# Kernel optimization log

Hardware: AMD Instinct MI355X
Metric: run time of the kernel (lower is better)

Reference implementation:

```python
import jax, jax.numpy as jnp
import numpy as np

B, S, H, I, G = 2, 1024, 1024, 4096, 8


def setup_inputs() -> dict:
    key = jax.random.key(0)
    k1, k2, k3, k4 = jax.random.split(key, 4)
    # kaiming-style scaled init (scale matters only for numerics, not math)
    hidden_states = jax.random.normal(k1, (B, S, H), dtype=jnp.float32)
    WG = jax.random.normal(k2, (H, G), dtype=jnp.float32) * (1.0 / np.sqrt(H))
    Wi = jax.random.normal(k3, (G, H, I), dtype=jnp.float32) * (1.0 / np.sqrt(H))
    down = jax.random.normal(k4, (I, H), dtype=jnp.float32) * (1.0 / np.sqrt(I))
    return {"hidden_states": hidden_states, "WG": WG, "Wi": Wi, "down": down, "topk": 2}


def topk_sigmoid(gate, k):
    # gate: [B,S,G] -> sigmoid gated scores masked to top-k per token
    _, idx = jax.lax.top_k(gate, k)                       # idx: [B,S,k]
    mask = (idx[..., None] == jnp.arange(gate.shape[-1])).any(axis=-2)  # [B,S,G] bool
    return jax.nn.sigmoid(gate) * mask


def reference(hidden_states, WG, Wi, down, topk):
    gate = hidden_states @ WG                             # [B,S,G]
    g = topk_sigmoid(gate, topk)                          # [B,S,G]
    # dense contraction over all groups (faithful to original einsum)
    up = jnp.einsum('bse,bsg,geo->bso', hidden_states, g, Wi)  # [B,S,I]
    act = jnp.square(jax.nn.relu(up))                     # ReLU^2
    return act @ down                                     # [B,S,H]
```

## Files before the change

kernel.cpp:

```cpp
#include <hip/hip_runtime.h>
#include <hip/hip_bf16.h>

typedef unsigned short u16;
typedef short short8_t __attribute__((ext_vector_type(8)));
typedef float f32x4 __attribute__((ext_vector_type(4)));

#define GLOBAL_AS(p) ((const __attribute__((address_space(1))) void*)(p))
#define LDS_AS(p)    ((__attribute__((address_space(3))) void*)(p))

__device__ __forceinline__ u16 f2bf(float f) {
    union { float f; unsigned int u; } x;
    x.f = f;
    unsigned int r = x.u + 0x7fffu + ((x.u >> 16) & 1u);
    return (u16)(r >> 16);
}

#define M_NMT   0
#define M_TE    2
#define M_TB    42
#define M_PAIR  96
#define M_RTOK  4192
#define M_RW    9312

__global__ __launch_bounds__(64) void gate_topk_kernel(
    const float* __restrict__ h, const float* __restrict__ wg, float* __restrict__ w) {
    const int t = blockIdx.x;
    const int lane = threadIdx.x;
    float acc[8];
#pragma unroll
    for (int g = 0; g < 8; ++g) acc[g] = 0.f;
    for (int e = lane; e < 1024; e += 64) {
        float hv = h[(size_t)t * 1024 + e];
        float4 r0 = *(const float4*)&wg[e * 8];
        float4 r1 = *(const float4*)&wg[e * 8 + 4];
        acc[0] += hv * r0.x; acc[1] += hv * r0.y; acc[2] += hv * r0.z; acc[3] += hv * r0.w;
        acc[4] += hv * r1.x; acc[5] += hv * r1.y; acc[6] += hv * r1.z; acc[7] += hv * r1.w;
    }
#pragma unroll
    for (int off = 32; off > 0; off >>= 1) {
#pragma unroll
        for (int g = 0; g < 8; ++g) acc[g] += __shfl_down(acc[g], off);
    }
    if (lane == 0) {
        int i1 = 0;
        for (int g = 1; g < 8; ++g) if (acc[g] > acc[i1]) i1 = g;
        int i2 = -1;
        for (int g = 0; g < 8; ++g) {
            if (g == i1) continue;
            if (i2 < 0 || acc[g] > acc[i2]) i2 = g;
        }
#pragma unroll
        for (int g = 0; g < 8; ++g) {
            float v = (g == i1 || g == i2) ? (1.f / (1.f + __expf(-acc[g]))) : 0.f;
            w[t * 8 + g] = v;
        }
    }
}

__global__ __launch_bounds__(256) void scan_kernel(
    const float* __restrict__ w, int* __restrict__ meta) {
    __shared__ int cnt[8], pos[8];
    const int tid = threadIdx.x;
    if (tid < 8) cnt[tid] = 0;
    __syncthreads();
    for (int t = tid; t < 2048; t += 256) {
#pragma unroll
        for (int g = 0; g < 8; ++g)
            if (w[t * 8 + g] > 0.f) atomicAdd(&cnt[g], 1);
    }
    __syncthreads();
    if (tid == 0) {
        int base = 0, mt = 0;
        for (int e = 0; e < 8; ++e) {
            pos[e] = base;
            int nt = (cnt[e] + 127) >> 7;
            for (int k = 0; k < nt; ++k) { meta[M_TE + mt] = e; meta[M_TB + mt] = base + k * 128; ++mt; }
            base += nt << 7;
        }
        meta[M_NMT] = mt;
        meta[1] = base;
    }
    __syncthreads();
    for (int i = tid; i < 5120; i += 256) meta[M_RTOK + i] = -1;
    __syncthreads();
    float* row_w = (float*)&meta[M_RW];
    for (int t = tid; t < 2048; t += 256) {
        int slot = 0;
#pragma unroll
        for (int g = 0; g < 8; ++g) {
            float wv = w[t * 8 + g];
            if (wv > 0.f) {
                int p = atomicAdd(&pos[g], 1);
                meta[M_RTOK + p] = t;
                row_w[p] = wv;
                meta[M_PAIR + t * 2 + slot] = p;
                ++slot;
            }
        }
    }
}

__global__ __launch_bounds__(256) void gather_a_kernel(
    const float* __restrict__ h, const int* __restrict__ meta, u16* __restrict__ A) {
    const int row = blockIdx.x;
    const int tid = threadIdx.x;
    const int tok = meta[M_RTOK + row];
    u16* dst = A + (size_t)row * 1024;
    if (tok < 0) {
        uint2 z; z.x = 0u; z.y = 0u;
        ((uint2*)dst)[tid] = z;
        return;
    }
    const float wv = ((const float*)&meta[M_RW])[row];
    float4 v = ((const float4*)(h + (size_t)tok * 1024))[tid];
    u16 o[4] = { f2bf(v.x * wv), f2bf(v.y * wv), f2bf(v.z * wv), f2bf(v.w * wv) };
    ((uint2*)dst)[tid] = *(const uint2*)o;
}

__global__ __launch_bounds__(256) void gemm1_sparse_kernel(
    const u16* __restrict__ A, const float* __restrict__ Wi,
    float* __restrict__ up, const int* __restrict__ meta) {
    const int mt = blockIdx.y;
    if (mt >= meta[M_NMT]) return;
    const int e = meta[M_TE + mt];
    const int base = meta[M_TB + mt];
    const int n0 = blockIdx.x * 128;
    const int K = 1024, N = 4096;
    const float* Bm = Wi + (size_t)e * K * N;

    __shared__ short a_tile[128 * 64];
    __shared__ short b_tile[128 * 64];
    const int tid = threadIdx.x;
    const int lane = tid & 63;
    const int wave = tid >> 6;
    const int wm = (wave >> 1) * 64;
    const int wn = (wave & 1) * 64;
    const int r = lane & 15;
    const int quad = lane >> 4;
    const int rowin = lane >> 3;
    const int achk = ((lane & 7) ^ (rowin & 7)) * 8;
    const int aldst = (lane & 7) * 8;

    const f32x4 vzero = {0.f, 0.f, 0.f, 0.f};
    f32x4 acc[4][4];
#pragma unroll
    for (int i = 0; i < 4; ++i)
#pragma unroll
        for (int j = 0; j < 4; ++j) acc[i][j] = vzero;

    for (int kb = 0; kb < K; kb += 64) {
        float bv[4][8];
#pragma unroll
        for (int cb = 0; cb < 4; ++cb) {
            int idx = cb * 256 + tid;
            int bn_ = idx & 127;
            int bk8 = idx >> 7;
            const float* bp = Bm + (size_t)(kb + bk8 * 8) * N + n0 + bn_;
#pragma unroll
            for (int kk = 0; kk < 8; ++kk) bv[cb][kk] = bp[(size_t)kk * N];
        }
        __syncthreads();
#pragma unroll
        for (int it = 0; it < 4; ++it) {
            int row = wave * 8 + it * 32 + rowin;
            const u16* ga = A + (size_t)(base + row) * K + kb + achk;
            __builtin_amdgcn_global_load_lds(GLOBAL_AS(ga), LDS_AS(&a_tile[row * 64 + aldst]), 16, 0, 0);
        }
#pragma unroll
        for (int cb = 0; cb < 4; ++cb) {
            int idx = cb * 256 + tid;
            int bn_ = idx & 127;
            int bk8 = idx >> 7;
            u16 bc[8];
#pragma unroll
            for (int kk = 0; kk < 8; ++kk) bc[kk] = f2bf(bv[cb][kk]);
            *(short8_t*)&b_tile[bn_ * 64 + ((bk8 ^ (bn_ & 7)) * 8)] = *(const short8_t*)bc;
        }
        __syncthreads();
#pragma unroll
        for (int ks = 0; ks < 2; ++ks) {
            const int cp = ((ks * 4 + quad) ^ (r & 7)) * 8;
            short8_t af[4], bfr[4];
#pragma unroll
            for (int i = 0; i < 4; ++i)
                af[i] = *(const short8_t*)&a_tile[(wm + i * 16 + r) * 64 + cp];
#pragma unroll
            for (int j = 0; j < 4; ++j)
                bfr[j] = *(const short8_t*)&b_tile[(wn + j * 16 + r) * 64 + cp];
#pragma unroll
            for (int i = 0; i < 4; ++i)
#pragma unroll
                for (int j = 0; j < 4; ++j)
                    acc[i][j] = __builtin_amdgcn_mfma_f32_16x16x32_bf16(af[i], bfr[j], acc[i][j], 0, 0, 0);
        }
        __syncthreads();
    }
#pragma unroll
    for (int i = 0; i < 4; ++i)
#pragma unroll
        for (int j = 0; j < 4; ++j)
#pragma unroll
            for (int reg = 0; reg < 4; ++reg) {
                int cr = base + wm + i * 16 + quad * 4 + reg;
                int cc = n0 + wn + j * 16 + r;
                up[(size_t)cr * N + cc] = acc[i][j][reg];
            }
}

__global__ __launch_bounds__(256) void combine_kernel(
    const float* __restrict__ up, const int* __restrict__ meta, u16* __restrict__ act) {
    const int t = blockIdx.x;
    const int tid = threadIdx.x;
    const int p0 = meta[M_PAIR + t * 2];
    const int p1 = meta[M_PAIR + t * 2 + 1];
    const float* r0 = up + (size_t)p0 * 4096;
    const float* r1 = up + (size_t)p1 * 4096;
    u16* dst = act + (size_t)t * 4096;
#pragma unroll
    for (int it = 0; it < 4; ++it) {
        int i = (tid + it * 256) * 4;
        float4 a = *(const float4*)&r0[i];
        float4 b = *(const float4*)&r1[i];
        float s0 = a.x + b.x, s1 = a.y + b.y, s2 = a.z + b.z, s3 = a.w + b.w;
        s0 = s0 > 0.f ? s0 * s0 : 0.f;
        s1 = s1 > 0.f ? s1 * s1 : 0.f;
        s2 = s2 > 0.f ? s2 * s2 : 0.f;
        s3 = s3 > 0.f ? s3 * s3 : 0.f;
        u16 o[4] = { f2bf(s0), f2bf(s1), f2bf(s2), f2bf(s3) };
        *(uint2*)&dst[i] = *(const uint2*)o;
    }
}

__global__ __launch_bounds__(256) void transpose_cvt_kernel(
    const float* __restrict__ in, u16* __restrict__ out, int R, int C) {
    __shared__ u16 tile[64][65];
    const int rt = blockIdx.y * 64;
    const int ct = blockIdx.x * 64;
    const int tid = threadIdx.x;
#pragma unroll
    for (int it = 0; it < 2; ++it) {
        int r = (tid >> 3) + it * 32;
        int c8 = (tid & 7) * 8;
        const float* ip = &in[(size_t)(rt + r) * C + ct + c8];
        float4 v0 = *(const float4*)ip;
        float4 v1 = *(const float4*)(ip + 4);
        tile[c8 + 0][r] = f2bf(v0.x); tile[c8 + 1][r] = f2bf(v0.y);
        tile[c8 + 2][r] = f2bf(v0.z); tile[c8 + 3][r] = f2bf(v0.w);
        tile[c8 + 4][r] = f2bf(v1.x); tile[c8 + 5][r] = f2bf(v1.y);
        tile[c8 + 6][r] = f2bf(v1.z); tile[c8 + 7][r] = f2bf(v1.w);
    }
    __syncthreads();
#pragma unroll
    for (int it = 0; it < 2; ++it) {
        int c = (tid >> 3) + it * 32;
        int r8 = (tid & 7) * 8;
        u16 tmp[8];
#pragma unroll
        for (int j = 0; j < 8; ++j) tmp[j] = tile[c][r8 + j];
        *(uint4*)&out[(size_t)(ct + c) * R + rt + r8] = *(const uint4*)tmp;
    }
}

template <int BM, int WROWS, int WCOLS>
__global__ __launch_bounds__(256) void gemm_tn_kernel(
    const u16* __restrict__ X, const u16* __restrict__ Y, float* __restrict__ Cout,
    int M, int N, int K) {
    constexpr int WM = BM / WROWS;
    constexpr int WN = 128 / WCOLS;
    constexpr int FI = WM / 16;
    constexpr int FJ = WN / 16;
    __shared__ short a_tile[BM * 64];
    __shared__ short b_tile[128 * 64];
    const int tid = threadIdx.x;
    const int lane = tid & 63;
    const int wave = tid >> 6;

    const int Nt = gridDim.x, Mt = gridDim.y;
    const int lid = blockIdx.y * Nt + blockIdx.x;
    const int xcd = lid & 7;
    const int p = lid >> 3;
    const int n_tile = xcd * (Nt >> 3) + p / Mt;
    const int m_tile = p % Mt;
    const int m0 = m_tile * BM;
    const int n0 = n_tile * 128;

    const int wm = (wave / WCOLS) * WM;
    const int wn = (wave % WCOLS) * WN;
    const int rowin = lane >> 3;
    const int achk = ((lane & 7) ^ (rowin & 7)) * 8;
    const int aldst = (lane & 7) * 8;
    const int r = lane & 15;
    const int quad = lane >> 4;

    const f32x4 vzero = {0.f, 0.f, 0.f, 0.f};
    f32x4 acc[FI][FJ];
#pragma unroll
    for (int i = 0; i < FI; ++i)
#pragma unroll
        for (int j = 0; j < FJ; ++j) acc[i][j] = vzero;

    for (int kb = 0; kb < K; kb += 64) {
#pragma unroll
        for (int it = 0; it < BM / 32; ++it) {
            int row = wave * 8 + it * 32 + rowin;
            const u16* ga = X + (size_t)(m0 + row) * K + kb + achk;
            __builtin_amdgcn_global_load_lds(GLOBAL_AS(ga), LDS_AS(&a_tile[row * 64 + aldst]), 16, 0, 0);
        }
#pragma unroll
        for (int it = 0; it < 4; ++it) {
            int row = wave * 8 + it * 32 + rowin;
            const u16* gb = Y + (size_t)(n0 + row) * K + kb + achk;
            __builtin_amdgcn_global_load_lds(GLOBAL_AS(gb), LDS_AS(&b_tile[row * 64 + aldst]), 16, 0, 0);
        }
        __syncthreads();
#pragma unroll
        for (int ks = 0; ks < 2; ++ks) {
            const int cp = ((ks * 4 + quad) ^ (r & 7)) * 8;
            short8_t af[FI], bfr[FJ];
#pragma unroll
            for (int i = 0; i < FI; ++i)
                af[i] = *(const short8_t*)&a_tile[(wm + i * 16 + r) * 64 + cp];
#pragma unroll
            for (int j = 0; j < FJ; ++j)
                bfr[j] = *(const short8_t*)&b_tile[(wn + j * 16 + r) * 64 + cp];
#pragma unroll
            for (int i = 0; i < FI; ++i)
#pragma unroll
                for (int j = 0; j < FJ; ++j)
                    acc[i][j] = __builtin_amdgcn_mfma_f32_16x16x32_bf16(af[i], bfr[j], acc[i][j], 0, 0, 0);
        }
        __syncthreads();
    }
#pragma unroll
    for (int i = 0; i < FI; ++i)
#pragma unroll
        for (int j = 0; j < FJ; ++j)
#pragma unroll
            for (int reg = 0; reg < 4; ++reg) {
                int cr = m0 + wm + i * 16 + quad * 4 + reg;
                int cc = n0 + wn + j * 16 + r;
                Cout[(size_t)cr * N + cc] = acc[i][j][reg];
            }
}

extern "C" void kernel_launch(void* const* d_in, const int* in_sizes, int n_in,
                              void* d_out, int out_size, void* d_ws, size_t ws_size,
                              hipStream_t stream) {
    const float* h    = (const float*)d_in[0];
    const float* WG   = (const float*)d_in[1];
    const float* Wi   = (const float*)d_in[2];
    const float* down = (const float*)d_in[3];
    float* out = (float*)d_out;

    const int T = 2048, H = 1024, I = 4096;

    char* ws = (char*)d_ws;
    float* w_gate = (float*)(ws);
    int*   meta   = (int*)(ws + 65536);
    u16*   Arow   = (u16*)(ws + 131072);
    float* up     = (float*)(ws + 131072 + 10485760);
    u16*   act    = (u16*)(ws + 131072 + 10485760 + 83886080);
    u16*   downT  = (u16*)(ws + 131072 + 10485760 + 83886080 + 16777216);

    gate_topk_kernel<<<T, 64, 0, stream>>>(h, WG, w_gate);
    scan_kernel<<<1, 256, 0, stream>>>(w_gate, meta);
    gather_a_kernel<<<5120, 256, 0, stream>>>(h, meta, Arow);

    gemm1_sparse_kernel<<<dim3(32, 40), 256, 0, stream>>>(Arow, Wi, up, meta);

    combine_kernel<<<T, 256, 0, stream>>>(up, meta, act);

    transpose_cvt_kernel<<<dim3(H / 64, I / 64), 256, 0, stream>>>(down, downT, I, H);
    gemm_tn_kernel<64, 1, 4><<<dim3(H / 128, T / 64), 256, 0, stream>>>(
        act, downT, out, T, H, I);
}
```

Before: 376.4 us.

## Double-buffer LDS tiles and prefetch next K-slab in both GEMM kernels

Both GEMM kernels now use ping-pong LDS buffers so the next K-slab's global-to-LDS loads are issued while the current slab is being multiplied. This removes one barrier per iteration. The sparse gemm1 kernel also holds two register sets of fp32 weights and loads two slabs ahead, with sched_barriers that pin the issue order, and gains a launch_bounds minimum of 2 blocks. The cost is twice the LDS per block and more registers, which may lower occupancy or cause spills.

```diff
diff --git a/kernel.cpp b/kernel.cpp
--- a/kernel.cpp
+++ b/kernel.cpp
@@ -117,7 +117,7 @@
     ((uint2*)dst)[tid] = *(const uint2*)o;
 }
 
-__global__ __launch_bounds__(256) void gemm1_sparse_kernel(
+__global__ __launch_bounds__(256, 2) void gemm1_sparse_kernel(
     const u16* __restrict__ A, const float* __restrict__ Wi,
     float* __restrict__ up, const int* __restrict__ meta) {
     const int mt = blockIdx.y;
@@ -128,8 +128,8 @@
     const int K = 1024, N = 4096;
     const float* Bm = Wi + (size_t)e * K * N;
 
-    __shared__ short a_tile[128 * 64];
-    __shared__ short b_tile[128 * 64];
+    __shared__ short a_tile[2][128 * 64];
+    __shared__ short b_tile[2][128 * 64];
     const int tid = threadIdx.x;
     const int lane = tid & 63;
     const int wave = tid >> 6;
@@ -140,6 +140,8 @@
     const int rowin = lane >> 3;
     const int achk = ((lane & 7) ^ (rowin & 7)) * 8;
     const int aldst = (lane & 7) * 8;
+    const int bidx_n = tid & 127;
+    const int bidx_k8 = tid >> 7;
 
     const f32x4 vzero = {0.f, 0.f, 0.f, 0.f};
     f32x4 acc[4][4];
@@ -148,53 +150,99 @@
 #pragma unroll
         for (int j = 0; j < 4; ++j) acc[i][j] = vzero;
 
-    for (int kb = 0; kb < K; kb += 64) {
-        float bv[4][8];
-#pragma unroll
-        for (int cb = 0; cb < 4; ++cb) {
-            int idx = cb * 256 + tid;
-            int bn_ = idx & 127;
-            int bk8 = idx >> 7;
-            const float* bp = Bm + (size_t)(kb + bk8 * 8) * N + n0 + bn_;
-#pragma unroll
-            for (int kk = 0; kk < 8; ++kk) bv[cb][kk] = bp[(size_t)kk * N];
+    float bvA[4][8], bvB[4][8];
+
+#define G1_LOADB(bv, kb_)                                                             \
+    {                                                                                 \
+        const int kbc = (kb_);                                                        \
+        _Pragma("unroll")                                                             \
+        for (int cb = 0; cb < 4; ++cb) {                                              \
+            const float* bp = Bm + (size_t)(kbc + (bidx_k8 + cb * 2) * 8) * N + n0 + bidx_n; \
+            _Pragma("unroll")                                                         \
+            for (int kk = 0; kk < 8; ++kk) bv[cb][kk] = bp[(size_t)kk * N];            \
+        }                                                                             \
+    }
+
+#define G1_STOREB(bv, buf)                                                            \
+    {                                                                                 \
+        _Pragma("unroll")                                                             \
+        for (int cb = 0; cb < 4; ++cb) {                                              \
+            int bk8 = bidx_k8 + cb * 2;                                               \
+            u16 bc[8];                                                                \
+            _Pragma("unroll")                                                         \
+            for (int kk = 0; kk < 8; ++kk) bc[kk] = f2bf(bv[cb][kk]);                  \
+            *(short8_t*)&b_tile[buf][bidx_n * 64 + ((bk8 ^ (bidx_n & 7)) * 8)] =       \
+                *(const short8_t*)bc;                                                 \
+        }                                                                             \
+    }
+
+#define G1_STAGEA(kb_, buf)                                                           \
+    {                                                                                 \
+        const int kbc = (kb_);                                                        \
+        _Pragma("unroll")                                                             \
+        for (int it = 0; it < 4; ++it) {                                              \
+            int row = wave * 8 + it * 32 + rowin;                                     \
+            const u16* ga = A + (size_t)(base + row) * K + kbc + achk;                \
+            __builtin_amdgcn_global_load_lds(GLOBAL_AS(ga),                           \
+                LDS_AS(&a_tile[buf][row * 64 + aldst]), 16, 0, 0);                    \
+        }                                                                             \
+    }
+
+#define G1_COMPUTE(buf)                                                               \
+    {                                                                                 \
+        _Pragma("unroll")                                                             \
+        for (int ks = 0; ks < 2; ++ks) {                                              \
+            const int cp = ((ks * 4 + quad) ^ (r & 7)) * 8;                           \
+            short8_t af[4], bfr[4];                                                   \
+            _Pragma("unroll")                                                         \
+            for (int i = 0; i < 4; ++i)                                               \
+                af[i] = *(const short8_t*)&a_tile[buf][(wm + i * 16 + r) * 64 + cp];  \
+            _Pragma("unroll")                                                         \
+            for (int j = 0; j < 4; ++j)                                               \
+                bfr[j] = *(const short8_t*)&b_tile[buf][(wn + j * 16 + r) * 64 + cp]; \
+            _Pragma("unroll")                                                         \
+            for (int i = 0; i < 4; ++i)                                               \
+                _Pragma("unroll")                                                     \
+                for (int j = 0; j < 4; ++j)                                           \
+                    acc[i][j] = __builtin_amdgcn_mfma_f32_16x16x32_bf16(              \
+                        af[i], bfr[j], acc[i][j], 0, 0, 0);                           \
+        }                                                                             \
+    }
+
+    G1_LOADB(bvA, 0);
+    G1_STAGEA(0, 0);
+    G1_STOREB(bvA, 0);
+    G1_LOADB(bvB, 64);
+    __syncthreads();
+
+    for (int t = 0; t < 14; t += 2) {
+        G1_LOADB(bvA, (t + 2) * 64);
+        __builtin_amdgcn_sched_barrier(0);
+        G1_STAGEA((t + 1) * 64, 1);
+        G1_STOREB(bvB, 1);
+        G1_COMPUTE(0);
+        __syncthreads();
+        {
+            int kbn = (t + 3) * 64; if (kbn > 960) kbn = 960;
+            G1_LOADB(bvB, kbn);
         }
+        __builtin_amdgcn_sched_barrier(0);
+        G1_STAGEA((t + 2) * 64, 0);
+        G1_STOREB(bvA, 0);
+        G1_COMPUTE(1);
         __syncthreads();
-#pragma unroll
-        for (int it = 0; it < 4; ++it) {
-            int row = wave * 8 + it * 32 + rowin;
-            const u16* ga = A + (size_t)(base + row) * K + kb + achk;
-            __builtin_amdgcn_global_load_lds(GLOBAL_AS(ga), LDS_AS(&a_tile[row * 64 + aldst]), 16, 0, 0);
-        }
-#pragma unroll
-        for (int cb = 0; cb < 4; ++cb) {
-            int idx = cb * 256 + tid;
-            int bn_ = idx & 127;
-            int bk8 = idx >> 7;
-            u16 bc[8];
-#pragma unroll
-            for (int kk = 0; kk < 8; ++kk) bc[kk] = f2bf(bv[cb][kk]);
-            *(short8_t*)&b_tile[bn_ * 64 + ((bk8 ^ (bn_ & 7)) * 8)] = *(const short8_t*)bc;
-        }
-        __syncthreads();
-#pragma unroll
-        for (int ks = 0; ks < 2; ++ks) {
-            const int cp = ((ks * 4 + quad) ^ (r & 7)) * 8;
-            short8_t af[4], bfr[4];
-#pragma unroll
-            for (int i = 0; i < 4; ++i)
-                af[i] = *(const short8_t*)&a_tile[(wm + i * 16 + r) * 64 + cp];
-#pragma unroll
-            for (int j = 0; j < 4; ++j)
-                bfr[j] = *(const short8_t*)&b_tile[(wn + j * 16 + r) * 64 + cp];
-#pragma unroll
-            for (int i = 0; i < 4; ++i)
-#pragma unroll
-                for (int j = 0; j < 4; ++j)
-                    acc[i][j] = __builtin_amdgcn_mfma_f32_16x16x32_bf16(af[i], bfr[j], acc[i][j], 0, 0, 0);
-        }
-        __syncthreads();
-    }
+    }
+    G1_STAGEA(960, 1);
+    G1_STOREB(bvB, 1);
+    G1_COMPUTE(0);
+    __syncthreads();
+    G1_COMPUTE(1);
+
+#undef G1_LOADB
+#undef G1_STOREB
+#undef G1_STAGEA
+#undef G1_COMPUTE
+
 #pragma unroll
     for (int i = 0; i < 4; ++i)
 #pragma unroll
@@ -269,8 +317,8 @@
     constexpr int WN = 128 / WCOLS;
     constexpr int FI = WM / 16;
     constexpr int FJ = WN / 16;
-    __shared__ short a_tile[BM * 64];
-    __shared__ short b_tile[128 * 64];
+    __shared__ short a_tile[2][BM * 64];
+    __shared__ short b_tile[2][128 * 64];
     const int tid = threadIdx.x;
     const int lane = tid & 63;
     const int wave = tid >> 6;
@@ -299,38 +347,60 @@
 #pragma unroll
         for (int j = 0; j < FJ; ++j) acc[i][j] = vzero;
 
-    for (int kb = 0; kb < K; kb += 64) {
-#pragma unroll
-        for (int it = 0; it < BM / 32; ++it) {
-            int row = wave * 8 + it * 32 + rowin;
-            const u16* ga = X + (size_t)(m0 + row) * K + kb + achk;
-            __builtin_amdgcn_global_load_lds(GLOBAL_AS(ga), LDS_AS(&a_tile[row * 64 + aldst]), 16, 0, 0);
-        }
-#pragma unroll
-        for (int it = 0; it < 4; ++it) {
-            int row = wave * 8 + it * 32 + rowin;
-            const u16* gb = Y + (size_t)(n0 + row) * K + kb + achk;
-            __builtin_amdgcn_global_load_lds(GLOBAL_AS(gb), LDS_AS(&b_tile[row * 64 + aldst]), 16, 0, 0);
-        }
+#define G2_STAGE(kb_, buf)                                                            \
+    {                                                                                 \
+        const int kbc = (kb_);                                                        \
+        _Pragma("unroll")                                                             \
+        for (int it = 0; it < BM / 32; ++it) {                                        \
+            int row = wave * 8 + it * 32 + rowin;                                     \
+            const u16* ga = X + (size_t)(m0 + row) * K + kbc + achk;                  \
+            __builtin_amdgcn_global_load_lds(GLOBAL_AS(ga),                           \
+                LDS_AS(&a_tile[buf][row * 64 + aldst]), 16, 0, 0);                    \
+        }                                                                             \
+        _Pragma("unroll")                                                             \
+        for (int it = 0; it < 4; ++it) {                                              \
+            int row = wave * 8 + it * 32 + rowin;                                     \
+            const u16* gb = Y + (size_t)(n0 + row) * K + kbc + achk;                  \
+            __builtin_amdgcn_global_load_lds(GLOBAL_AS(gb),                           \
+                LDS_AS(&b_tile[buf][row * 64 + aldst]), 16, 0, 0);                    \
+        }                                                                             \
+    }
+
+#define G2_COMPUTE(buf)                                                               \
+    {                                                                                 \
+        _Pragma("unroll")                                                             \
+        for (int ks = 0; ks < 2; ++ks) {                                              \
+            const int cp = ((ks * 4 + quad) ^ (r & 7)) * 8;                           \
+            short8_t af[FI], bfr[FJ];                                                 \
+            _Pragma("unroll")                                                         \
+            for (int i = 0; i < FI; ++i)                                              \
+                af[i] = *(const short8_t*)&a_tile[buf][(wm + i * 16 + r) * 64 + cp];  \
+            _Pragma("unroll")                                                         \
+            for (int j = 0; j < FJ; ++j)                                              \
+                bfr[j] = *(const short8_t*)&b_tile[buf][(wn + j * 16 + r) * 64 + cp]; \
+            _Pragma("unroll")                                                         \
+            for (int i = 0; i < FI; ++i)                                              \
+                _Pragma("unroll")                                                     \
+                for (int j = 0; j < FJ; ++j)                                          \
+                    acc[i][j] = __builtin_amdgcn_mfma_f32_16x16x32_bf16(              \
+                        af[i], bfr[j], acc[i][j], 0, 0, 0);                           \
+        }                                                                             \
+    }
+
+    const int nk = K >> 6;
+    G2_STAGE(0, 0);
+    __syncthreads();
+    for (int t = 0; t < nk - 1; ++t) {
+        const int nxt = (t + 1) & 1;
+        G2_STAGE((t + 1) * 64, nxt);
+        G2_COMPUTE(t & 1);
         __syncthreads();
-#pragma unroll
-        for (int ks = 0; ks < 2; ++ks) {
-            const int cp = ((ks * 4 + quad) ^ (r & 7)) * 8;
-            short8_t af[FI], bfr[FJ];
-#pragma unroll
-            for (int i = 0; i < FI; ++i)
-                af[i] = *(const short8_t*)&a_tile[(wm + i * 16 + r) * 64 + cp];
-#pragma unroll
-            for (int j = 0; j < FJ; ++j)
-                bfr[j] = *(const short8_t*)&b_tile[(wn + j * 16 + r) * 64 + cp];
-#pragma unroll
-            for (int i = 0; i < FI; ++i)
-#pragma unroll
-                for (int j = 0; j < FJ; ++j)
-                    acc[i][j] = __builtin_amdgcn_mfma_f32_16x16x32_bf16(af[i], bfr[j], acc[i][j], 0, 0, 0);
-        }
-        __syncthreads();
-    }
+    }
+    G2_COMPUTE((nk - 1) & 1);
+
+#undef G2_STAGE
+#undef G2_COMPUTE
+
 #pragma unroll
     for (int i = 0; i < FI; ++i)
 #pragma unroll
```

Measured after the change: 393.4 us. +4.5%, slower.
